# Optimization experiments

Measured on AMD Instinct MI355X. Metric: run time of the kernel, lower is better.

The kernel has to match this reference:

```python
import jax, jax.numpy as jnp
import numpy as np

N = 50000
E = 600000
D_IN = 128
D_OUT = 128
EPS = 1e-12  # F.normalize eps


def setup_inputs() -> dict:
    key = jax.random.key(0)
    ks = jax.random.split(key, 10)
    s = 1.0 / np.sqrt(D_IN)
    inp = {
        "x": jax.random.normal(ks[0], (N, D_IN), dtype=jnp.float32),
        "edge_index": jax.random.randint(ks[1], (2, E), 0, N, dtype=jnp.int64),
        # conv1: lin_l (with bias) applied to aggregated neighbors, lin_r (no bias) to root
        "W1l": jax.random.uniform(ks[2], (D_IN, D_IN), jnp.float32, -s, s),
        "b1": jax.random.uniform(ks[3], (D_IN,), jnp.float32, -s, s),
        "W1r": jax.random.uniform(ks[4], (D_IN, D_IN), jnp.float32, -s, s),
        # conv2
        "W2l": jax.random.uniform(ks[5], (D_IN, D_OUT), jnp.float32, -s, s),
        "b2": jax.random.uniform(ks[6], (D_OUT,), jnp.float32, -s, s),
        "W2r": jax.random.uniform(ks[7], (D_IN, D_OUT), jnp.float32, -s, s),
        # final fc
        "Wf": jax.random.uniform(ks[8], (D_OUT, D_OUT), jnp.float32, -s, s),
        "bf": jax.random.uniform(ks[9], (D_OUT,), jnp.float32, -s, s),
    }
    return inp


def _sage_conv(x, src, dst, Wl, bl, Wr):
    # mean-aggregate messages from source nodes onto destination nodes
    msgs = x[src]  # [E, d] gather
    agg = jax.ops.segment_sum(msgs, dst, num_segments=N)  # [N, d]
    cnt = jax.ops.segment_sum(jnp.ones((src.shape[0],), x.dtype), dst, num_segments=N)
    agg = agg / jnp.maximum(cnt, 1.0)[:, None]  # isolated nodes -> 0
    out = agg @ Wl + bl + x @ Wr
    # L2 normalize per node (PyG normalize=True)
    nrm = jnp.sqrt(jnp.sum(out * out, axis=-1, keepdims=True))
    return out / jnp.maximum(nrm, EPS)


def reference(x, edge_index, W1l, b1, W1r, W2l, b2, W2r, Wf, bf):
    src, dst = edge_index[0], edge_index[1]
    h = jax.nn.relu(_sage_conv(x, src, dst, W1l, b1, W1r))
    h = jax.nn.relu(_sage_conv(h, src, dst, W2l, b2, W2r))
    return h @ Wf + bf
```

## Files before the change

### kernel.cpp

```cpp
#include <hip/hip_runtime.h>
#include <hip/hip_fp16.h>

#define D 128
#define SCAN_B 256
#define HLD 136

typedef __attribute__((ext_vector_type(8))) _Float16 f16x8;
typedef __attribute__((ext_vector_type(4))) float f32x4;

__global__ void scan_pass1(const int* __restrict__ cnt, int* __restrict__ rs,
                           int* __restrict__ bsum, int N) {
    __shared__ int lds[SCAN_B];
    int tid = threadIdx.x;
    int i = blockIdx.x * SCAN_B + tid;
    int v = (i < N) ? cnt[i] : 0;
    lds[tid] = v;
    __syncthreads();
    for (int o = 1; o < SCAN_B; o <<= 1) {
        int t = (tid >= o) ? lds[tid - o] : 0;
        __syncthreads();
        lds[tid] += t;
        __syncthreads();
    }
    if (i < N) rs[i] = lds[tid] - v;
    if (tid == SCAN_B - 1) bsum[blockIdx.x] = lds[tid];
}

__global__ void scan_pass2(int* __restrict__ bsum, int nb) {
    __shared__ int lds[SCAN_B];
    int tid = threadIdx.x;
    int v = (tid < nb) ? bsum[tid] : 0;
    lds[tid] = v;
    __syncthreads();
    for (int o = 1; o < SCAN_B; o <<= 1) {
        int t = (tid >= o) ? lds[tid - o] : 0;
        __syncthreads();
        lds[tid] += t;
        __syncthreads();
    }
    if (tid < nb) bsum[tid] = lds[tid] - v;
}

__global__ void scan_pass3(int* __restrict__ rs, int* __restrict__ cursor,
                           const int* __restrict__ bsum, const int* __restrict__ cnt,
                           float* __restrict__ inv, int N) {
    int i = blockIdx.x * SCAN_B + threadIdx.x;
    if (i < N) {
        int v = rs[i] + bsum[blockIdx.x];
        rs[i] = v;
        cursor[i] = v;
        inv[i] = 1.0f / (float)max(cnt[i], 1);
    }
}

__global__ void fill_kernel(const int* __restrict__ ei, int E,
                            int* __restrict__ cursor, int* __restrict__ csr) {
    int e = blockIdx.x * blockDim.x + threadIdx.x;
    if (e < E) {
        int src = ei[e], dst = ei[E + e];
        int pos = atomicAdd(&cursor[dst], 1);
        csr[pos] = src;
    }
}

__global__ void prologue_kernel(const float* __restrict__ W1l, const float* __restrict__ W1r,
                                const float* __restrict__ W2l, const float* __restrict__ W2r,
                                const float* __restrict__ Wf, unsigned short* __restrict__ pw,
                                const float* __restrict__ x, __half* __restrict__ xh, int n8,
                                const int* __restrict__ ei, int E, int* __restrict__ cnt) {
    int t = blockIdx.x * blockDim.x + threadIdx.x;
    if (t < 10240) {
        int idx = t;
        int w = idx >> 11;
        int r = idx & 2047;
        int ks = r >> 9;
        int tt = (r >> 6) & 7;
        int lane = r & 63;
        int q = lane >> 4, n = lane & 15;
        const float* W = (w == 0) ? W1l : (w == 1) ? W1r : (w == 2) ? W2l : (w == 3) ? W2r : Wf;
        unsigned short* dh = pw + (size_t)w * 32768;
        unsigned short* dl = dh + 16384;
        int off = ((ks * 8 + tt) * 64 + lane) * 8;
#pragma unroll
        for (int j = 0; j < 8; j++) {
            float v = W[(size_t)(ks * 32 + q * 8 + j) * D + tt * 16 + n];
            __half hb = __float2half_rn(v);
            dh[off + j] = __half_as_ushort(hb);
            dl[off + j] = __half_as_ushort(__float2half_rn(v - __half2float(hb)));
        }
    } else if (t < 10240 + n8) {
        int i = t - 10240;
        const float4* x4 = (const float4*)x;
        float4 a = x4[2 * i], b = x4[2 * i + 1];
        __half2 h0 = __floats2half2_rn(a.x, a.y);
        __half2 h1 = __floats2half2_rn(a.z, a.w);
        __half2 h2 = __floats2half2_rn(b.x, b.y);
        __half2 h3 = __floats2half2_rn(b.z, b.w);
        uint4 o;
        o.x = *(const unsigned*)&h0;
        o.y = *(const unsigned*)&h1;
        o.z = *(const unsigned*)&h2;
        o.w = *(const unsigned*)&h3;
        ((uint4*)xh)[i] = o;
    } else {
        int e = t - 10240 - n8;
        if (e < E) atomicAdd(&cnt[ei[E + e]], 1);
    }
}

__device__ __forceinline__ void acc8(uint4 v, float* s) {
    const __half2* h = reinterpret_cast<const __half2*>(&v);
    float2 f0 = __half22float2(h[0]);
    float2 f1 = __half22float2(h[1]);
    float2 f2 = __half22float2(h[2]);
    float2 f3 = __half22float2(h[3]);
    s[0] += f0.x; s[1] += f0.y; s[2] += f1.x; s[3] += f1.y;
    s[4] += f2.x; s[5] += f2.y; s[6] += f3.x; s[7] += f3.y;
}

__global__ void aggregate_kernel(const __half* __restrict__ xh, int sstride,
                                 const int* __restrict__ csr,
                                 const int* __restrict__ rs, const int* __restrict__ cnt,
                                 const float* __restrict__ inv,
                                 __half* __restrict__ aggh, __half* __restrict__ aggl, int N) {
    int t = blockIdx.x * blockDim.x + threadIdx.x;
    int node = t >> 4;
    int c = t & 15;
    if (node >= N) return;
    int deg = cnt[node];
    int st = rs[node];
    const uint4* x4 = (const uint4*)xh;
    float s[8] = {0.f, 0.f, 0.f, 0.f, 0.f, 0.f, 0.f, 0.f};
    int i = 0;
    for (; i + 4 <= deg; i += 4) {
        int n0 = csr[st + i + 0], n1 = csr[st + i + 1];
        int n2 = csr[st + i + 2], n3 = csr[st + i + 3];
        uint4 v0 = x4[(size_t)n0 * sstride + c];
        uint4 v1 = x4[(size_t)n1 * sstride + c];
        uint4 v2 = x4[(size_t)n2 * sstride + c];
        uint4 v3 = x4[(size_t)n3 * sstride + c];
        acc8(v0, s); acc8(v1, s); acc8(v2, s); acc8(v3, s);
    }
    for (; i < deg; i++) {
        int n0 = csr[st + i];
        uint4 v0 = x4[(size_t)n0 * sstride + c];
        acc8(v0, s);
    }
    float iv = inv[node];
    uint4 oh, ol;
    __half2* ph = (__half2*)&oh;
    __half2* pl = (__half2*)&ol;
#pragma unroll
    for (int jj = 0; jj < 4; jj++) {
        float v0 = s[2 * jj] * iv, v1 = s[2 * jj + 1] * iv;
        __half h0 = __float2half_rn(v0), h1 = __float2half_rn(v1);
        ph[jj] = __halves2half2(h0, h1);
        pl[jj] = __halves2half2(__float2half_rn(v0 - __half2float(h0)),
                                __float2half_rn(v1 - __half2float(h1)));
    }
    ((uint4*)aggh)[(size_t)node * 16 + c] = oh;
    ((uint4*)aggl)[(size_t)node * 16 + c] = ol;
}

__device__ __forceinline__ void split_f16(const float* v, uint4& hi, uint4& lo) {
    __half2* ph = (__half2*)&hi;
    __half2* pl = (__half2*)&lo;
#pragma unroll
    for (int jj = 0; jj < 4; jj++) {
        __half h0 = __float2half_rn(v[2 * jj]);
        __half h1 = __float2half_rn(v[2 * jj + 1]);
        ph[jj] = __halves2half2(h0, h1);
        pl[jj] = __halves2half2(__float2half_rn(v[2 * jj] - __half2float(h0)),
                                __float2half_rn(v[2 * jj + 1] - __half2float(h1)));
    }
}

template <int LAYER>
__global__ __launch_bounds__(256) void mfma_gemm(
        const uint4* __restrict__ Agh, const uint4* __restrict__ Agl,
        const float* __restrict__ Xf,
        const uint4* Hio,
        const uint4* __restrict__ W0h, const uint4* __restrict__ W0l,
        const uint4* __restrict__ W1h, const uint4* __restrict__ W1l,
        const float* __restrict__ bias,
        const uint4* __restrict__ W2h, const uint4* __restrict__ W2l,
        const float* __restrict__ bias2,
        float* out, __half* Hout, int N) {
    __shared__ __half Hs[(LAYER == 2) ? 4 * 2 * 16 * HLD : 4];

    const int tid = threadIdx.x;
    const int lane = tid & 63;
    const int wave = tid >> 6;
    const int c = lane & 15;
    const int q = lane >> 4;
    const int R = blockIdx.x * 64 + wave * 16;
    const int row0 = min(R + c, N - 1);

    uint4 Ah_[8], Al_[8];
    const size_t rb16 = (size_t)row0 * 16 + q;
#pragma unroll
    for (int kl = 0; kl < 4; kl++) {
        Ah_[kl] = Agh[rb16 + kl * 4];
        Al_[kl] = Agl[rb16 + kl * 4];
    }
    if (LAYER == 1) {
        const float4* xf4 = (const float4*)Xf;
        const size_t xb = (size_t)row0 * 32 + q * 2;
        float4 xa[8];
#pragma unroll
        for (int kl = 0; kl < 4; kl++) {
            xa[2 * kl] = xf4[xb + kl * 8];
            xa[2 * kl + 1] = xf4[xb + kl * 8 + 1];
        }
#pragma unroll
        for (int kl = 0; kl < 4; kl++) {
            float v[8] = {xa[2 * kl].x, xa[2 * kl].y, xa[2 * kl].z, xa[2 * kl].w,
                          xa[2 * kl + 1].x, xa[2 * kl + 1].y, xa[2 * kl + 1].z, xa[2 * kl + 1].w};
            split_f16(v, Ah_[4 + kl], Al_[4 + kl]);
        }
    } else {
        const size_t rb32 = (size_t)row0 * 32 + q;
#pragma unroll
        for (int kl = 0; kl < 4; kl++) {
            Ah_[4 + kl] = Hio[rb32 + kl * 4];
            Al_[4 + kl] = Hio[rb32 + 16 + kl * 4];
        }
    }

    uint4 wh[2][8], wl[2][8];
#pragma unroll
    for (int t = 0; t < 8; t++) {
        wh[0][t] = W0h[(size_t)t * 64 + lane];
        wl[0][t] = W0l[(size_t)t * 64 + lane];
    }

    f32x4 acc[8];
#pragma unroll
    for (int t = 0; t < 8; t++)
#pragma unroll
        for (int r = 0; r < 4; r++) acc[t][r] = 0.0f;

#pragma unroll
    for (int ks = 0; ks < 8; ks++) {
        if (ks < 7) {
            const uint4* Whn = (((ks + 1) < 4) ? W0h : W1h) + (size_t)((ks + 1) & 3) * 512 + lane;
            const uint4* Wln = (((ks + 1) < 4) ? W0l : W1l) + (size_t)((ks + 1) & 3) * 512 + lane;
#pragma unroll
            for (int t = 0; t < 8; t++) {
                wh[(ks + 1) & 1][t] = Whn[t * 64];
                wl[(ks + 1) & 1][t] = Wln[t * 64];
            }
        }
        f16x8 ah = __builtin_bit_cast(f16x8, Ah_[ks]);
        f16x8 al = __builtin_bit_cast(f16x8, Al_[ks]);
#pragma unroll
        for (int t = 0; t < 8; t++) {
            f16x8 bh = __builtin_bit_cast(f16x8, wh[ks & 1][t]);
            f16x8 bl = __builtin_bit_cast(f16x8, wl[ks & 1][t]);
            acc[t] = __builtin_amdgcn_mfma_f32_16x16x32_f16(ah, bh, acc[t], 0, 0, 0);
            acc[t] = __builtin_amdgcn_mfma_f32_16x16x32_f16(al, bh, acc[t], 0, 0, 0);
            acc[t] = __builtin_amdgcn_mfma_f32_16x16x32_f16(ah, bl, acc[t], 0, 0, 0);
        }
    }

#pragma unroll
    for (int t = 0; t < 8; t++) {
        float bv = bias[t * 16 + c];
#pragma unroll
        for (int r = 0; r < 4; r++) acc[t][r] += bv;
    }
#pragma unroll
    for (int r = 0; r < 4; r++) {
        float v = 0.0f;
#pragma unroll
        for (int t = 0; t < 8; t++) v += acc[t][r] * acc[t][r];
        v += __shfl_xor(v, 1, 16);
        v += __shfl_xor(v, 2, 16);
        v += __shfl_xor(v, 4, 16);
        v += __shfl_xor(v, 8, 16);
        float rn = 1.0f / fmaxf(sqrtf(v), 1e-12f);
#pragma unroll
        for (int t = 0; t < 8; t++) acc[t][r] = fmaxf(acc[t][r] * rn, 0.0f);
    }

    if (LAYER == 1) {
#pragma unroll
        for (int t = 0; t < 8; t++)
#pragma unroll
            for (int r = 0; r < 4; r++) {
                int row = R + q * 4 + r;
                if (row < N) {
                    float v = acc[t][r];
                    __half h = __float2half_rn(v);
                    size_t base = (size_t)row * 256;
                    Hout[base + t * 16 + c] = h;
                    Hout[base + 128 + t * 16 + c] = __float2half_rn(v - __half2float(h));
                }
            }
        return;
    }

    uint4 w2h[2][8], w2l[2][8];
#pragma unroll
    for (int t = 0; t < 8; t++) {
        w2h[0][t] = W2h[(size_t)t * 64 + lane];
        w2l[0][t] = W2l[(size_t)t * 64 + lane];
    }

    __half* hh = &Hs[wave * (2 * 16 * HLD)];
    __half* hl = hh + 16 * HLD;
#pragma unroll
    for (int t = 0; t < 8; t++)
#pragma unroll
        for (int r = 0; r < 4; r++) {
            int m = q * 4 + r;
            float v = acc[t][r];
            __half h = __float2half_rn(v);
            hh[m * HLD + t * 16 + c] = h;
            hl[m * HLD + t * 16 + c] = __float2half_rn(v - __half2float(h));
        }
    __syncthreads();

    uint4 a2h_[4], a2l_[4];
#pragma unroll
    for (int k2 = 0; k2 < 4; k2++) {
        a2h_[k2] = *(const uint4*)&hh[c * HLD + k2 * 32 + q * 8];
        a2l_[k2] = *(const uint4*)&hl[c * HLD + k2 * 32 + q * 8];
    }

    f32x4 acc2[8];
#pragma unroll
    for (int t = 0; t < 8; t++) {
        float bv = bias2[t * 16 + c];
#pragma unroll
        for (int r = 0; r < 4; r++) acc2[t][r] = bv;
    }
#pragma unroll
    for (int k2 = 0; k2 < 4; k2++) {
        if (k2 < 3) {
            const uint4* Whn = W2h + (size_t)(k2 + 1) * 512 + lane;
            const uint4* Wln = W2l + (size_t)(k2 + 1) * 512 + lane;
#pragma unroll
            for (int t = 0; t < 8; t++) {
                w2h[(k2 + 1) & 1][t] = Whn[t * 64];
                w2l[(k2 + 1) & 1][t] = Wln[t * 64];
            }
        }
        f16x8 ah = __builtin_bit_cast(f16x8, a2h_[k2]);
        f16x8 al = __builtin_bit_cast(f16x8, a2l_[k2]);
#pragma unroll
        for (int t = 0; t < 8; t++) {
            f16x8 bh = __builtin_bit_cast(f16x8, w2h[k2 & 1][t]);
            f16x8 bl = __builtin_bit_cast(f16x8, w2l[k2 & 1][t]);
            acc2[t] = __builtin_amdgcn_mfma_f32_16x16x32_f16(ah, bh, acc2[t], 0, 0, 0);
            acc2[t] = __builtin_amdgcn_mfma_f32_16x16x32_f16(al, bh, acc2[t], 0, 0, 0);
            acc2[t] = __builtin_amdgcn_mfma_f32_16x16x32_f16(ah, bl, acc2[t], 0, 0, 0);
        }
    }

#pragma unroll
    for (int t = 0; t < 8; t++)
#pragma unroll
        for (int r = 0; r < 4; r++) {
            int row = R + q * 4 + r;
            if (row < N) out[(size_t)row * D + t * 16 + c] = acc2[t][r];
        }
}

extern "C" void kernel_launch(void* const* d_in, const int* in_sizes, int n_in,
                              void* d_out, int out_size, void* d_ws, size_t ws_size,
                              hipStream_t stream) {
    const float* x   = (const float*)d_in[0];
    const int*   ei  = (const int*)d_in[1];
    const float* W1l = (const float*)d_in[2];
    const float* b1  = (const float*)d_in[3];
    const float* W1r = (const float*)d_in[4];
    const float* W2l = (const float*)d_in[5];
    const float* b2  = (const float*)d_in[6];
    const float* W2r = (const float*)d_in[7];
    const float* Wf  = (const float*)d_in[8];
    const float* bf  = (const float*)d_in[9];
    float* out = (float*)d_out;

    int N = in_sizes[0] / D;
    int E = in_sizes[1] / 2;

    __half* Agh = (__half*)d_ws;
    __half* Agl = Agh + (size_t)N * D;
    __half* Xh  = Agl + (size_t)N * D;
    float* inv  = (float*)(Xh + (size_t)N * D);
    int*   rs     = (int*)(inv + N);
    int*   cnt    = rs + N;
    int*   cursor = cnt + N;
    int*   bsum   = cursor + N;
    int*   csr    = bsum + 256;
    unsigned short* pw = (unsigned short*)(csr + E);
    unsigned short* p1lh = pw + 0 * 32768, *p1ll = p1lh + 16384;
    unsigned short* p1rh = pw + 1 * 32768, *p1rl = p1rh + 16384;
    unsigned short* p2lh = pw + 2 * 32768, *p2ll = p2lh + 16384;
    unsigned short* p2rh = pw + 3 * 32768, *p2rl = p2rh + 16384;
    unsigned short* pfh  = pw + 4 * 32768, *pfl  = pfh + 16384;

    __half* H1 = (__half*)d_out;

    int nb = (N + SCAN_B - 1) / SCAN_B;
    int n8 = N * 16;

    hipMemsetAsync(cnt, 0, (size_t)N * sizeof(int), stream);
    int pro_threads = 10240 + n8 + E;
    prologue_kernel<<<(pro_threads + 255) / 256, 256, 0, stream>>>(
        W1l, W1r, W2l, W2r, Wf, pw, x, Xh, n8, ei, E, cnt);
    scan_pass1<<<nb, SCAN_B, 0, stream>>>(cnt, rs, bsum, N);
    scan_pass2<<<1, SCAN_B, 0, stream>>>(bsum, nb);
    scan_pass3<<<nb, SCAN_B, 0, stream>>>(rs, cursor, bsum, cnt, inv, N);
    fill_kernel<<<(E + 255) / 256, 256, 0, stream>>>(ei, E, cursor, csr);

    int agg_blocks = (N * 16 + 255) / 256;
    int gemm_blocks = (N + 63) / 64;

    aggregate_kernel<<<agg_blocks, 256, 0, stream>>>(Xh, 16, csr, rs, cnt, inv, Agh, Agl, N);
    mfma_gemm<1><<<gemm_blocks, 256, 0, stream>>>(
        (const uint4*)Agh, (const uint4*)Agl, x, nullptr,
        (const uint4*)p1lh, (const uint4*)p1ll, (const uint4*)p1rh, (const uint4*)p1rl, b1,
        nullptr, nullptr, nullptr, nullptr, H1, N);

    aggregate_kernel<<<agg_blocks, 256, 0, stream>>>(H1, 32, csr, rs, cnt, inv, Agh, Agl, N);
    mfma_gemm<2><<<gemm_blocks, 256, 0, stream>>>(
        (const uint4*)Agh, (const uint4*)Agl, nullptr, (const uint4*)d_out,
        (const uint4*)p2lh, (const uint4*)p2ll, (const uint4*)p2rh, (const uint4*)p2rl, b2,
        (const uint4*)pfh, (const uint4*)pfl, bf, out, nullptr, N);
}
```

Measured before the change: 287.3 us.

## Stage GEMM weight slabs through shared LDS instead of per-wave global loads

Each of the four waves used to load every weight slab from global memory into its own registers. Now the block loads each slab once, split across waves, into double-buffered LDS, and every wave reads the B fragments from there. A operands are also loaded one k-step at a time instead of all up front. This cuts global/L2 traffic and register pressure, but adds per-k-step __syncthreads barriers and larger LDS use (32–50 KB), which may lower occupancy.

```diff
diff --git a/kernel.cpp b/kernel.cpp
--- a/kernel.cpp
+++ b/kernel.cpp
@@ -175,6 +175,19 @@
     }
 }
 
+__device__ __forceinline__ void w_issue(const uint4* __restrict__ srch,
+                                        const uint4* __restrict__ srcl,
+                                        int wave, int lane, uint4* st) {
+    const uint4* src = ((wave < 2) ? srch : srcl) + ((wave & 1) * 256 + lane);
+#pragma unroll
+    for (int i = 0; i < 4; i++) st[i] = src[i * 64];
+}
+__device__ __forceinline__ void w_commit(char* dstbase, int wave, int lane, const uint4* st) {
+    uint4* dst = (uint4*)(dstbase + wave * 4096 + lane * 16);
+#pragma unroll
+    for (int i = 0; i < 4; i++) dst[i * 64] = st[i];
+}
+
 template <int LAYER>
 __global__ __launch_bounds__(256) void mfma_gemm(
         const uint4* __restrict__ Agh, const uint4* __restrict__ Agl,
@@ -186,7 +199,8 @@
         const uint4* __restrict__ W2h, const uint4* __restrict__ W2l,
         const float* __restrict__ bias2,
         float* out, __half* Hout, int N) {
-    __shared__ __half Hs[(LAYER == 2) ? 4 * 2 * 16 * HLD : 4];
+    __shared__ uint4 smem4[(LAYER == 2 ? 51200 : 32768) / 16];
+    char* smem = (char*)smem4;
 
     const int tid = threadIdx.x;
     const int lane = tid & 63;
@@ -195,44 +209,33 @@
     const int q = lane >> 4;
     const int R = blockIdx.x * 64 + wave * 16;
     const int row0 = min(R + c, N - 1);
-
-    uint4 Ah_[8], Al_[8];
     const size_t rb16 = (size_t)row0 * 16 + q;
-#pragma unroll
-    for (int kl = 0; kl < 4; kl++) {
-        Ah_[kl] = Agh[rb16 + kl * 4];
-        Al_[kl] = Agl[rb16 + kl * 4];
-    }
-    if (LAYER == 1) {
-        const float4* xf4 = (const float4*)Xf;
-        const size_t xb = (size_t)row0 * 32 + q * 2;
-        float4 xa[8];
-#pragma unroll
-        for (int kl = 0; kl < 4; kl++) {
-            xa[2 * kl] = xf4[xb + kl * 8];
-            xa[2 * kl + 1] = xf4[xb + kl * 8 + 1];
-        }
-#pragma unroll
-        for (int kl = 0; kl < 4; kl++) {
-            float v[8] = {xa[2 * kl].x, xa[2 * kl].y, xa[2 * kl].z, xa[2 * kl].w,
-                          xa[2 * kl + 1].x, xa[2 * kl + 1].y, xa[2 * kl + 1].z, xa[2 * kl + 1].w};
-            split_f16(v, Ah_[4 + kl], Al_[4 + kl]);
-        }
-    } else {
-        const size_t rb32 = (size_t)row0 * 32 + q;
-#pragma unroll
-        for (int kl = 0; kl < 4; kl++) {
-            Ah_[4 + kl] = Hio[rb32 + kl * 4];
-            Al_[4 + kl] = Hio[rb32 + 16 + kl * 4];
-        }
-    }
-
-    uint4 wh[2][8], wl[2][8];
-#pragma unroll
-    for (int t = 0; t < 8; t++) {
-        wh[0][t] = W0h[(size_t)t * 64 + lane];
-        wl[0][t] = W0l[(size_t)t * 64 + lane];
-    }
+
+    auto wsrc_h = [&](int ks) { return ((ks < 4) ? W0h : W1h) + (size_t)(ks & 3) * 512; };
+    auto wsrc_l = [&](int ks) { return ((ks < 4) ? W0l : W1l) + (size_t)(ks & 3) * 512; };
+    auto load_a = [&](int ks, uint4& ah, uint4& al) {
+        if (ks < 4) {
+            ah = Agh[rb16 + ks * 4];
+            al = Agl[rb16 + ks * 4];
+        } else if (LAYER == 1) {
+            const float4* xf4 = (const float4*)Xf;
+            size_t xb = (size_t)row0 * 32 + q * 2 + (size_t)(ks - 4) * 8;
+            float4 xa = xf4[xb], xb2 = xf4[xb + 1];
+            float v[8] = {xa.x, xa.y, xa.z, xa.w, xb2.x, xb2.y, xb2.z, xb2.w};
+            split_f16(v, ah, al);
+        } else {
+            size_t rb32 = (size_t)row0 * 32 + q + (size_t)(ks - 4) * 4;
+            ah = Hio[rb32];
+            al = Hio[rb32 + 16];
+        }
+    };
+
+    uint4 st[4];
+    uint4 A_h[2], A_l[2];
+    w_issue(wsrc_h(0), wsrc_l(0), wave, lane, st);
+    load_a(0, A_h[0], A_l[0]);
+    w_commit(smem, wave, lane, st);
+    __syncthreads();
 
     f32x4 acc[8];
 #pragma unroll
@@ -242,25 +245,24 @@
 
 #pragma unroll
     for (int ks = 0; ks < 8; ks++) {
+        const int b = ks & 1;
         if (ks < 7) {
-            const uint4* Whn = (((ks + 1) < 4) ? W0h : W1h) + (size_t)((ks + 1) & 3) * 512 + lane;
-            const uint4* Wln = (((ks + 1) < 4) ? W0l : W1l) + (size_t)((ks + 1) & 3) * 512 + lane;
-#pragma unroll
-            for (int t = 0; t < 8; t++) {
-                wh[(ks + 1) & 1][t] = Whn[t * 64];
-                wl[(ks + 1) & 1][t] = Wln[t * 64];
-            }
-        }
-        f16x8 ah = __builtin_bit_cast(f16x8, Ah_[ks]);
-        f16x8 al = __builtin_bit_cast(f16x8, Al_[ks]);
+            w_issue(wsrc_h(ks + 1), wsrc_l(ks + 1), wave, lane, st);
+            load_a(ks + 1, A_h[b ^ 1], A_l[b ^ 1]);
+        }
+        const uint4* wb = (const uint4*)(smem + b * 16384);
+        f16x8 ah = __builtin_bit_cast(f16x8, A_h[b]);
+        f16x8 al = __builtin_bit_cast(f16x8, A_l[b]);
 #pragma unroll
         for (int t = 0; t < 8; t++) {
-            f16x8 bh = __builtin_bit_cast(f16x8, wh[ks & 1][t]);
-            f16x8 bl = __builtin_bit_cast(f16x8, wl[ks & 1][t]);
+            f16x8 bh = __builtin_bit_cast(f16x8, wb[t * 64 + lane]);
+            f16x8 bl = __builtin_bit_cast(f16x8, wb[512 + t * 64 + lane]);
             acc[t] = __builtin_amdgcn_mfma_f32_16x16x32_f16(ah, bh, acc[t], 0, 0, 0);
             acc[t] = __builtin_amdgcn_mfma_f32_16x16x32_f16(al, bh, acc[t], 0, 0, 0);
             acc[t] = __builtin_amdgcn_mfma_f32_16x16x32_f16(ah, bl, acc[t], 0, 0, 0);
         }
+        if (ks < 7) w_commit(smem + (b ^ 1) * 16384, wave, lane, st);
+        __syncthreads();
     }
 
 #pragma unroll
@@ -300,14 +302,10 @@
         return;
     }
 
-    uint4 w2h[2][8], w2l[2][8];
-#pragma unroll
-    for (int t = 0; t < 8; t++) {
-        w2h[0][t] = W2h[(size_t)t * 64 + lane];
-        w2l[0][t] = W2l[(size_t)t * 64 + lane];
-    }
-
-    __half* hh = &Hs[wave * (2 * 16 * HLD)];
+    uint4 stf[4];
+    w_issue(W2h, W2l, wave, lane, stf);
+
+    __half* hh = (__half*)smem + wave * (2 * 16 * HLD);
     __half* hl = hh + 16 * HLD;
 #pragma unroll
     for (int t = 0; t < 8; t++)
@@ -319,6 +317,8 @@
             hh[m * HLD + t * 16 + c] = h;
             hl[m * HLD + t * 16 + c] = __float2half_rn(v - __half2float(h));
         }
+    char* wfb = smem + 34816;
+    w_commit(wfb, wave, lane, stf);
     __syncthreads();
 
     uint4 a2h_[4], a2l_[4];
@@ -335,26 +335,25 @@
 #pragma unroll
         for (int r = 0; r < 4; r++) acc2[t][r] = bv;
     }
+    const uint4* wb2 = (const uint4*)wfb;
 #pragma unroll
     for (int k2 = 0; k2 < 4; k2++) {
-        if (k2 < 3) {
-            const uint4* Whn = W2h + (size_t)(k2 + 1) * 512 + lane;
-            const uint4* Wln = W2l + (size_t)(k2 + 1) * 512 + lane;
-#pragma unroll
-            for (int t = 0; t < 8; t++) {
-                w2h[(k2 + 1) & 1][t] = Whn[t * 64];
-                w2l[(k2 + 1) & 1][t] = Wln[t * 64];
-            }
-        }
+        if (k2 < 3) w_issue(W2h + (size_t)(k2 + 1) * 512, W2l + (size_t)(k2 + 1) * 512,
+                            wave, lane, stf);
         f16x8 ah = __builtin_bit_cast(f16x8, a2h_[k2]);
         f16x8 al = __builtin_bit_cast(f16x8, a2l_[k2]);
 #pragma unroll
         for (int t = 0; t < 8; t++) {
-            f16x8 bh = __builtin_bit_cast(f16x8, w2h[k2 & 1][t]);
-            f16x8 bl = __builtin_bit_cast(f16x8, w2l[k2 & 1][t]);
+            f16x8 bh = __builtin_bit_cast(f16x8, wb2[t * 64 + lane]);
+            f16x8 bl = __builtin_bit_cast(f16x8, wb2[512 + t * 64 + lane]);
             acc2[t] = __builtin_amdgcn_mfma_f32_16x16x32_f16(ah, bh, acc2[t], 0, 0, 0);
             acc2[t] = __builtin_amdgcn_mfma_f32_16x16x32_f16(al, bh, acc2[t], 0, 0, 0);
             acc2[t] = __builtin_amdgcn_mfma_f32_16x16x32_f16(ah, bl, acc2[t], 0, 0, 0);
+        }
+        if (k2 < 3) {
+            __syncthreads();
+            w_commit(wfb, wave, lane, stf);
+            __syncthreads();
         }
     }
 
```

Result: slower. 310.3 us (+8.0%).
